# Kernel tuning notes

Measured on AMD Instinct MI355X. Metric: run time of the kernel, lower is better.

Reference implementation:

```python
import jax, jax.numpy as jnp
import numpy as np

N_NODES = 50000
N_EDGES = 800000
N_GRAPHS = 50
D_IN = 128
D_HID = 128
D_OUT = 10


def setup_inputs() -> dict:
    key = jax.random.key(0)
    ks = jax.random.split(key, 8)
    h = jax.random.normal(ks[0], (N_NODES, D_IN), dtype=jnp.float32)
    src = jax.random.randint(ks[1], (N_EDGES,), 0, N_NODES, dtype=jnp.int32)
    dst = jax.random.randint(ks[2], (N_EDGES,), 0, N_NODES, dtype=jnp.int32)
    graph_ids = jnp.sort(jax.random.randint(ks[3], (N_NODES,), 0, N_GRAPHS, dtype=jnp.int32))
    s = 1.0 / np.sqrt(D_HID)
    W1 = jax.random.normal(ks[4], (D_IN, D_HID), dtype=jnp.float32) * s
    W2 = jax.random.normal(ks[5], (D_HID, D_HID), dtype=jnp.float32) * s
    W3 = jax.random.normal(ks[6], (D_HID, D_HID), dtype=jnp.float32) * s
    Wm = jax.random.normal(ks[7], (D_HID, D_OUT), dtype=jnp.float32) * s
    return {
        "h": h, "src": src, "dst": dst, "graph_ids": graph_ids,
        "W1": W1, "b1": jnp.zeros((D_HID,), jnp.float32),
        "W2": W2, "b2": jnp.zeros((D_HID,), jnp.float32),
        "W3": W3, "b3": jnp.zeros((D_HID,), jnp.float32),
        "Wm": Wm, "bm": jnp.zeros((D_OUT,), jnp.float32),
    }


def _graph_conv(h, W, b, src, dst, norm_src, norm_dst):
    # DGL GraphConv, norm='both': out = D_dst^{-1/2} * A @ (D_src^{-1/2} * h) @ W + b
    m = (h * norm_src[:, None])[src]              # [E, d] gather (memory-bound)
    agg = jax.ops.segment_sum(m, dst, num_segments=N_NODES)  # [N, d] scatter-add
    return (agg * norm_dst[:, None]) @ W + b


def reference(h, src, dst, graph_ids, W1, b1, W2, b2, W3, b3, Wm, bm):
    ones_e = jnp.ones((N_EDGES,), jnp.float32)
    out_deg = jax.ops.segment_sum(ones_e, src, num_segments=N_NODES)
    in_deg = jax.ops.segment_sum(ones_e, dst, num_segments=N_NODES)
    norm_src = jnp.clip(out_deg, 1.0, None) ** -0.5
    norm_dst = jnp.clip(in_deg, 1.0, None) ** -0.5

    h = jax.nn.relu(_graph_conv(h, W1, b1, src, dst, norm_src, norm_dst))
    h = jax.nn.relu(_graph_conv(h, W2, b2, src, dst, norm_src, norm_dst))
    h = jax.nn.relu(_graph_conv(h, W3, b3, src, dst, norm_src, norm_dst))

    # mean-nodes readout per graph
    hg_sum = jax.ops.segment_sum(h, graph_ids, num_segments=N_GRAPHS)  # [G, d]
    cnt = jax.ops.segment_sum(jnp.ones((N_NODES,), jnp.float32), graph_ids, num_segments=N_GRAPHS)
    hg = hg_sum / jnp.clip(cnt, 1.0, None)[:, None]

    logits = hg @ Wm + bm                                 # [G, D_OUT]
    return jax.nn.log_softmax(logits, axis=0)             # faithful to dim=0 in source
```

## Files before the change

kernel.cpp:

```cpp
#include <hip/hip_runtime.h>

#define N_NODES 50000
#define N_EDGES 800000
#define N_GRAPHS 50
#define D 128
#define D_OUT 10
#define PLANE_F4 200000
#define NB 196
#define NBLK 196
#define AST 68
#define ZWORDS 50576

__global__ __launch_bounds__(256) void part_hist(const int* __restrict__ dst,
                                                 int* __restrict__ gh,
                                                 int* __restrict__ zbuf) {
    __shared__ int lh[NB];
    int tid = threadIdx.x, blk = blockIdx.x;
    int z = blk * 256 + tid;
    if (z < ZWORDS) zbuf[z] = 0;
    z += 50176;
    if (z < ZWORDS) zbuf[z] = 0;
    if (tid < NB) lh[tid] = 0;
    __syncthreads();
    int base = blk * 4096;
    #pragma unroll
    for (int j = 0; j < 16; j++) {
        int i = base + j * 256 + tid;
        if (i < N_EDGES) atomicAdd(&lh[dst[i] >> 8], 1);
    }
    __syncthreads();
    if (tid < NB) gh[tid * NBLK + blk] = lh[tid];
}

__global__ __launch_bounds__(1024) void part_scan(int* __restrict__ gh, int N) {
    __shared__ int wsum[16];
    __shared__ int carry_s;
    int tid = threadIdx.x;
    int lane = tid & 63, wid = tid >> 6;
    if (tid == 0) carry_s = 0;
    __syncthreads();
    for (int base = 0; base < N; base += 4096) {
        int i0 = base + tid * 4;
        int v0 = (i0 + 0 < N) ? gh[i0 + 0] : 0;
        int v1 = (i0 + 1 < N) ? gh[i0 + 1] : 0;
        int v2 = (i0 + 2 < N) ? gh[i0 + 2] : 0;
        int v3 = (i0 + 3 < N) ? gh[i0 + 3] : 0;
        int s = v0 + v1 + v2 + v3;
        int x = s;
        #pragma unroll
        for (int d = 1; d < 64; d <<= 1) {
            int y = __shfl_up(x, d, 64);
            if (lane >= d) x += y;
        }
        if (lane == 63) wsum[wid] = x;
        __syncthreads();
        if (wid == 0) {
            int t = (lane < 16) ? wsum[lane] : 0;
            #pragma unroll
            for (int d = 1; d < 16; d <<= 1) {
                int y = __shfl_up(t, d, 64);
                if (lane >= d) t += y;
            }
            if (lane < 16) wsum[lane] = t;
        }
        __syncthreads();
        int woff = (wid == 0) ? 0 : wsum[wid - 1];
        int run = carry_s + woff + (x - s);
        if (i0 + 0 < N) gh[i0 + 0] = run; run += v0;
        if (i0 + 1 < N) gh[i0 + 1] = run; run += v1;
        if (i0 + 2 < N) gh[i0 + 2] = run; run += v2;
        if (i0 + 3 < N) gh[i0 + 3] = run; run += v3;
        __syncthreads();
        if (tid == 0) carry_s += wsum[15];
        __syncthreads();
    }
}

__global__ __launch_bounds__(256) void part_scatter(const int* __restrict__ src,
                                                    const int* __restrict__ dst,
                                                    const int* __restrict__ gh,
                                                    unsigned int* __restrict__ packed,
                                                    int* __restrict__ out_deg) {
    __shared__ int lc[NB];
    int tid = threadIdx.x, blk = blockIdx.x;
    if (tid < NB) lc[tid] = gh[tid * NBLK + blk];
    __syncthreads();
    int base = blk * 4096;
    #pragma unroll
    for (int j = 0; j < 16; j++) {
        int i = base + j * 256 + tid;
        if (i < N_EDGES) {
            int d = dst[i];
            int s = src[i];
            atomicAdd(&out_deg[s], 1);
            int p = atomicAdd(&lc[d >> 8], 1);
            packed[p] = ((unsigned int)(d & 255) << 16) | (unsigned int)s;
        }
    }
}

__global__ __launch_bounds__(256) void bucket_csr(const unsigned int* __restrict__ packed,
                                                  const int* __restrict__ gh,
                                                  unsigned short* __restrict__ col16,
                                                  int* __restrict__ row_ptr,
                                                  float* __restrict__ nd,
                                                  int* __restrict__ dhb) {
    __shared__ unsigned int ep[8192];
    __shared__ unsigned short lcol[8192];
    __shared__ int hist[256], cur[256], wsum[4], ldh[64];
    int t = threadIdx.x, b = blockIdx.x;
    int nb = gh[b * NBLK];
    int ne = (b < NB - 1) ? gh[(b + 1) * NBLK] : N_EDGES;
    int cnt = ne - nb;
    if (cnt > 8192) cnt = 8192;
    hist[t] = 0;
    if (t < 64) ldh[t] = 0;
    __syncthreads();
    for (int i = t; i < cnt; i += 256) {
        unsigned int e = packed[nb + i];
        ep[i] = e;
        atomicAdd(&hist[e >> 16], 1);
    }
    __syncthreads();
    int v = hist[t];
    int lane = t & 63, w = t >> 6;
    int x = v;
    #pragma unroll
    for (int d = 1; d < 64; d <<= 1) {
        int y = __shfl_up(x, d, 64);
        if (lane >= d) x += y;
    }
    if (lane == 63) wsum[w] = x;
    __syncthreads();
    int add = 0;
    #pragma unroll
    for (int i = 0; i < 4; i++) if (i < w) add += wsum[i];
    int excl = add + x - v;
    cur[t] = excl;
    int node = b * 256 + t;
    if (node < N_NODES) {
        row_ptr[node] = nb + excl;
        int id = v > 1 ? v : 1;
        nd[node] = 1.0f / sqrtf((float)id);
        atomicAdd(&ldh[v < 63 ? v : 63], 1);
    }
    if (b == NB - 1 && t == 0) row_ptr[N_NODES] = N_EDGES;
    __syncthreads();
    if (t < 64) dhb[t * NBLK + b] = ldh[t];
    for (int i = t; i < cnt; i += 256) {
        unsigned int e = ep[i];
        int p = atomicAdd(&cur[e >> 16], 1);
        lcol[p] = (unsigned short)(e & 0xFFFF);
    }
    __syncthreads();
    for (int i = t; i < cnt; i += 256) col16[nb + i] = lcol[i];
}

__global__ __launch_bounds__(256) void dsort_scatter(const int* __restrict__ row_ptr,
                                                     const int* __restrict__ dhb,
                                                     int* __restrict__ perm) {
    __shared__ int lc[64];
    int t = threadIdx.x, b = blockIdx.x;
    if (t < 64) lc[t] = dhb[t * NBLK + b];
    __syncthreads();
    int n = b * 256 + t;
    if (n < N_NODES) {
        int deg = row_ptr[n + 1] - row_ptr[n];
        int bin = deg < 63 ? deg : 63;
        int pos = atomicAdd(&lc[bin], 1);
        perm[pos] = n;
    }
}

__global__ __launch_bounds__(256) void prescale_k(const float* __restrict__ h,
                                                  const int* __restrict__ out_deg,
                                                  float* __restrict__ out) {
    int i = blockIdx.x * 256 + threadIdx.x;
    if (i < N_NODES * 32) {
        int node = i >> 5;
        int kg = i & 31;
        float4 v = ((const float4*)h)[i];
        int od = out_deg[node];
        float s = 1.0f / sqrtf((float)(od > 1 ? od : 1));
        int p = kg >> 2, q = kg & 3;
        ((float4*)out)[p * PLANE_F4 + node * 4 + q] =
            make_float4(v.x * s, v.y * s, v.z * s, v.w * s);
    }
}

__global__ __launch_bounds__(256) void spmm_k(const float* __restrict__ x,
                                              const int* __restrict__ row_ptr,
                                              const unsigned short* __restrict__ col,
                                              const float* __restrict__ nd,
                                              const int* __restrict__ perm,
                                              float* __restrict__ out) {
    int b = blockIdx.x;
    int slice = b & 7;
    int idx = (b >> 3) * 64 + (threadIdx.x >> 2);
    if (idx >= N_NODES) return;
    int node = perm[idx];
    int q = threadIdx.x & 3;
    int s = row_ptr[node];
    int e = row_ptr[node + 1];
    const float4* xp = (const float4*)x + slice * PLANE_F4;
    float4 a0 = make_float4(0.f, 0.f, 0.f, 0.f);
    float4 a1 = make_float4(0.f, 0.f, 0.f, 0.f);
    float4 a2 = make_float4(0.f, 0.f, 0.f, 0.f);
    float4 a3 = make_float4(0.f, 0.f, 0.f, 0.f);
    int i = s;
    for (; i + 8 <= e; i += 8) {
        int c0 = col[i],     c1 = col[i + 1], c2 = col[i + 2], c3 = col[i + 3];
        int c4 = col[i + 4], c5 = col[i + 5], c6 = col[i + 6], c7 = col[i + 7];
        float4 h0 = xp[c0 * 4 + q];
        float4 h1 = xp[c1 * 4 + q];
        float4 h2 = xp[c2 * 4 + q];
        float4 h3 = xp[c3 * 4 + q];
        float4 h4 = xp[c4 * 4 + q];
        float4 h5 = xp[c5 * 4 + q];
        float4 h6 = xp[c6 * 4 + q];
        float4 h7 = xp[c7 * 4 + q];
        a0.x += h0.x; a0.y += h0.y; a0.z += h0.z; a0.w += h0.w;
        a1.x += h1.x; a1.y += h1.y; a1.z += h1.z; a1.w += h1.w;
        a2.x += h2.x; a2.y += h2.y; a2.z += h2.z; a2.w += h2.w;
        a3.x += h3.x; a3.y += h3.y; a3.z += h3.z; a3.w += h3.w;
        a0.x += h4.x; a0.y += h4.y; a0.z += h4.z; a0.w += h4.w;
        a1.x += h5.x; a1.y += h5.y; a1.z += h5.z; a1.w += h5.w;
        a2.x += h6.x; a2.y += h6.y; a2.z += h6.z; a2.w += h6.w;
        a3.x += h7.x; a3.y += h7.y; a3.z += h7.z; a3.w += h7.w;
    }
    for (; i + 4 <= e; i += 4) {
        int c0 = col[i], c1 = col[i + 1], c2 = col[i + 2], c3 = col[i + 3];
        float4 h0 = xp[c0 * 4 + q];
        float4 h1 = xp[c1 * 4 + q];
        float4 h2 = xp[c2 * 4 + q];
        float4 h3 = xp[c3 * 4 + q];
        a0.x += h0.x; a0.y += h0.y; a0.z += h0.z; a0.w += h0.w;
        a1.x += h1.x; a1.y += h1.y; a1.z += h1.z; a1.w += h1.w;
        a2.x += h2.x; a2.y += h2.y; a2.z += h2.z; a2.w += h2.w;
        a3.x += h3.x; a3.y += h3.y; a3.z += h3.z; a3.w += h3.w;
    }
    for (; i < e; i++) {
        float4 hv = xp[col[i] * 4 + q];
        a0.x += hv.x; a0.y += hv.y; a0.z += hv.z; a0.w += hv.w;
    }
    float ndv = nd[node];
    ((float4*)out)[slice * PLANE_F4 + node * 4 + q] =
        make_float4((a0.x + a1.x + a2.x + a3.x) * ndv,
                    (a0.y + a1.y + a2.y + a3.y) * ndv,
                    (a0.z + a1.z + a2.z + a3.z) * ndv,
                    (a0.w + a1.w + a2.w + a3.w) * ndv);
}

template <int MODE>
__global__ __launch_bounds__(128) void gemm_relu_k(const float* __restrict__ A,
                                                   const float* __restrict__ W,
                                                   const float* __restrict__ bias,
                                                   const int* __restrict__ odeg,
                                                   float* __restrict__ out) {
    __shared__ float As_t[128 * AST];
    int tid = threadIdx.x;
    int row0 = blockIdx.x * 64;
    const float4* A4 = (const float4*)A;
    const float4* W4 = (const float4*)W;

    #pragma unroll
    for (int it = 0; it < 16; it++) {
        int linear = it * 128 + tid;
        int p = linear >> 8;
        int rem = linear & 255;
        int r = rem >> 2;
        int q = rem & 3;
        int row = row0 + r;
        float4 a = (row < N_NODES) ? A4[p * PLANE_F4 + row * 4 + q]
                                   : make_float4(0.f, 0.f, 0.f, 0.f);
        int kb = p * 16 + q * 4;
        As_t[(kb + 0) * AST + r] = a.x;
        As_t[(kb + 1) * AST + r] = a.y;
        As_t[(kb + 2) * AST + r] = a.z;
        As_t[(kb + 3) * AST + r] = a.w;
    }
    __syncthreads();

    int tc = tid & 15;
    int tr = tid >> 4;
    float acc[8][8];
    #pragma unroll
    for (int r = 0; r < 8; r++)
        #pragma unroll
        for (int c = 0; c < 8; c++) acc[r][c] = 0.f;

    const float4* Wp = W4 + tc * 2;
    const float*  Ab = As_t + tr * 8;

    for (int k0 = 0; k0 < 128; k0 += 4) {
        float4 wv0[4], wv1[4], av0[4], av1[4];
        #pragma unroll
        for (int u = 0; u < 4; u++) {
            wv0[u] = Wp[(k0 + u) * 32];
            wv1[u] = Wp[(k0 + u) * 32 + 1];
        }
        #pragma unroll
        for (int u = 0; u < 4; u++) {
            av0[u] = *(const float4*)(Ab + (k0 + u) * AST);
            av1[u] = *(const float4*)(Ab + (k0 + u) * AST + 4);
        }
        #pragma unroll
        for (int u = 0; u < 4; u++) {
            float av[8] = {av0[u].x, av0[u].y, av0[u].z, av0[u].w,
                           av1[u].x, av1[u].y, av1[u].z, av1[u].w};
            float wv[8] = {wv0[u].x, wv0[u].y, wv0[u].z, wv0[u].w,
                           wv1[u].x, wv1[u].y, wv1[u].z, wv1[u].w};
            #pragma unroll
            for (int rr = 0; rr < 8; rr++)
                #pragma unroll
                for (int cc = 0; cc < 8; cc++)
                    acc[rr][cc] = fmaf(av[rr], wv[cc], acc[rr][cc]);
        }
    }

    float4 bv0 = ((const float4*)bias)[tc * 2];
    float4 bv1 = ((const float4*)bias)[tc * 2 + 1];
    #pragma unroll
    for (int rr = 0; rr < 8; rr++) {
        int row = row0 + tr * 8 + rr;
        if (row < N_NODES) {
            float4 o0, o1;
            o0.x = fmaxf(acc[rr][0] + bv0.x, 0.f);
            o0.y = fmaxf(acc[rr][1] + bv0.y, 0.f);
            o0.z = fmaxf(acc[rr][2] + bv0.z, 0.f);
            o0.w = fmaxf(acc[rr][3] + bv0.w, 0.f);
            o1.x = fmaxf(acc[rr][4] + bv1.x, 0.f);
            o1.y = fmaxf(acc[rr][5] + bv1.y, 0.f);
            o1.z = fmaxf(acc[rr][6] + bv1.z, 0.f);
            o1.w = fmaxf(acc[rr][7] + bv1.w, 0.f);
            if (MODE == 0) {
                int od = odeg[row];
                float s = 1.0f / sqrtf((float)(od > 1 ? od : 1));
                o0.x *= s; o0.y *= s; o0.z *= s; o0.w *= s;
                o1.x *= s; o1.y *= s; o1.z *= s; o1.w *= s;
                int p = tc >> 1;
                int q0 = (tc & 1) * 2;
                ((float4*)out)[p * PLANE_F4 + row * 4 + q0] = o0;
                ((float4*)out)[p * PLANE_F4 + row * 4 + q0 + 1] = o1;
            } else {
                ((float4*)out)[row * 32 + tc * 2] = o0;
                ((float4*)out)[row * 32 + tc * 2 + 1] = o1;
            }
        }
    }
}

__global__ __launch_bounds__(256) void proj_readout_k(const float* __restrict__ h,
                                                      const int* __restrict__ gid,
                                                      const float* __restrict__ Wm,
                                                      float* __restrict__ hgp,
                                                      int* __restrict__ gcnt) {
    __shared__ float Wmt[10 * 144];
    int tid = threadIdx.x;
    for (int i = tid; i < 1280; i += 256) {
        int k = i / 10, o = i % 10;
        Wmt[o * 144 + k + 4 * (k >> 5)] = Wm[i];
    }
    __syncthreads();

    int v = blockIdx.x * 64 + (tid >> 2);
    int quarter = tid & 3;
    int lane = tid & 63;

    float acc[D_OUT];
    #pragma unroll
    for (int o = 0; o < D_OUT; o++) acc[o] = 0.f;
    int g = -1;
    int cnt = 0;
    if (v < N_NODES) {
        g = gid[v];
        cnt = (quarter == 0) ? 1 : 0;
        const float4* h4 = (const float4*)h + v * 32 + quarter * 8;
        const float* wbase = Wmt + quarter * 36;
        #pragma unroll
        for (int kk = 0; kk < 8; kk++) {
            float4 hv = h4[kk];
            #pragma unroll
            for (int o = 0; o < D_OUT; o++) {
                float4 w = *(const float4*)(wbase + o * 144 + kk * 4);
                acc[o] += hv.x * w.x + hv.y * w.y + hv.z * w.z + hv.w * w.w;
            }
        }
    }

    #pragma unroll
    for (int d = 1; d < 64; d <<= 1) {
        int gp = __shfl_up(g, d, 64);
        int cp = __shfl_up(cnt, d, 64);
        bool take = (lane >= d) && (gp == g);
        #pragma unroll
        for (int o = 0; o < D_OUT; o++) {
            float ap = __shfl_up(acc[o], d, 64);
            if (take) acc[o] += ap;
        }
        if (take) cnt += cp;
    }
    int gn = __shfl_down(g, 1, 64);
    bool tail = (lane == 63) || (gn != g);
    if (tail && g >= 0) {
        #pragma unroll
        for (int o = 0; o < D_OUT; o++) atomicAdd(&hgp[g * D_OUT + o], acc[o]);
        if (cnt > 0) atomicAdd(&gcnt[g], cnt);
    }
}

__global__ __launch_bounds__(512) void final_k(const float* __restrict__ hgp,
                                               const int* __restrict__ gcnt,
                                               const float* __restrict__ bm,
                                               float* __restrict__ out) {
    __shared__ float lg[N_GRAPHS * D_OUT];
    __shared__ float colm[D_OUT], colls[D_OUT];
    int tid = threadIdx.x;
    if (tid < N_GRAPHS * D_OUT) {
        int g = tid / D_OUT, o = tid % D_OUT;
        float c = (float)gcnt[g];
        lg[tid] = hgp[tid] / (c > 1.f ? c : 1.f) + bm[o];
    }
    __syncthreads();
    if (tid < D_OUT) {
        float m = -1e30f;
        for (int g = 0; g < N_GRAPHS; g++) m = fmaxf(m, lg[g * D_OUT + tid]);
        float s = 0.f;
        for (int g = 0; g < N_GRAPHS; g++) s += expf(lg[g * D_OUT + tid] - m);
        colm[tid] = m; colls[tid] = logf(s);
    }
    __syncthreads();
    if (tid < N_GRAPHS * D_OUT) {
        int o = tid % D_OUT;
        out[tid] = lg[tid] - colm[o] - colls[o];
    }
}

extern "C" void kernel_launch(void* const* d_in, const int* in_sizes, int n_in,
                              void* d_out, int out_size, void* d_ws, size_t ws_size,
                              hipStream_t stream) {
    const float* h_in = (const float*)d_in[0];
    const int*   src  = (const int*)d_in[1];
    const int*   dst  = (const int*)d_in[2];
    const int*   gid  = (const int*)d_in[3];
    const float* W1 = (const float*)d_in[4];  const float* b1 = (const float*)d_in[5];
    const float* W2 = (const float*)d_in[6];  const float* b2 = (const float*)d_in[7];
    const float* W3 = (const float*)d_in[8];  const float* b3 = (const float*)d_in[9];
    const float* Wm = (const float*)d_in[10]; const float* bm = (const float*)d_in[11];

    char* ws = (char*)d_ws;
    int*            row_ptr = (int*)(ws + 0);
    unsigned short* col16   = (unsigned short*)(ws + 200032);
    float*          nd      = (float*)(ws + 1800032);
    int*            out_deg = (int*)(ws + 2000032);
    int*            gcnt    = (int*)(ws + 2200032);
    float*          hgp     = (float*)(ws + 2200288);
    int*            gh      = (int*)(ws + 2202336);
    int*            dhb     = (int*)(ws + 2356000);
    int*            perm    = (int*)(ws + 2406176);
    float*          bufA    = (float*)(ws + 2606176);
    float*          bufB    = (float*)(ws + 28206176);
    unsigned int*   packed  = (unsigned int*)bufB;

    part_hist<<<NBLK, 256, 0, stream>>>(dst, gh, out_deg);
    part_scan<<<1, 1024, 0, stream>>>(gh, NB * NBLK);
    part_scatter<<<NBLK, 256, 0, stream>>>(src, dst, gh, packed, out_deg);
    bucket_csr<<<NB, 256, 0, stream>>>(packed, gh, col16, row_ptr, nd, dhb);
    part_scan<<<1, 1024, 0, stream>>>(dhb, 64 * NBLK);
    dsort_scatter<<<196, 256, 0, stream>>>(row_ptr, dhb, perm);
    prescale_k<<<6250, 256, 0, stream>>>(h_in, out_deg, bufA);

    spmm_k<<<6256, 256, 0, stream>>>(bufA, row_ptr, col16, nd, perm, bufB);
    gemm_relu_k<0><<<782, 128, 0, stream>>>(bufB, W1, b1, out_deg, bufA);
    spmm_k<<<6256, 256, 0, stream>>>(bufA, row_ptr, col16, nd, perm, bufB);
    gemm_relu_k<0><<<782, 128, 0, stream>>>(bufB, W2, b2, out_deg, bufA);
    spmm_k<<<6256, 256, 0, stream>>>(bufA, row_ptr, col16, nd, perm, bufB);
    gemm_relu_k<1><<<782, 128, 0, stream>>>(bufB, W3, b3, out_deg, bufA);

    proj_readout_k<<<782, 256, 0, stream>>>(bufA, gid, Wm, hgp, gcnt);
    final_k<<<1, 512, 0, stream>>>(hgp, gcnt, bm, (float*)d_out);
}
```

Measured before the change: 525.6 us.

## Reorder CSR columns into degree-sorted order and stage them in LDS for SpMM

Adds a second row pointer array built by scanning per-position degrees in the degree-sorted permutation order. A new col_reorder kernel rewrites the column indices so each 64-row SpMM block reads a contiguous span. spmm_k now loads that span into shared memory cooperatively before gathering, and falls back to global reads when the span exceeds the LDS capacity. It also recomputes the dst norm from the degree instead of loading nd. The cost is two extra preprocessing launches (a scan and the reorder) plus an LDS staging pass and a barrier in each SpMM block.

```diff
diff --git a/kernel.cpp b/kernel.cpp
--- a/kernel.cpp
+++ b/kernel.cpp
@@ -9,6 +9,7 @@
 #define NB 196
 #define NBLK 196
 #define AST 68
+#define LCOL_CAP 3072
 #define ZWORDS 50576
 
 __global__ __launch_bounds__(256) void part_hist(const int* __restrict__ dst,
@@ -103,7 +104,6 @@
                                                   const int* __restrict__ gh,
                                                   unsigned short* __restrict__ col16,
                                                   int* __restrict__ row_ptr,
-                                                  float* __restrict__ nd,
                                                   int* __restrict__ dhb) {
     __shared__ unsigned int ep[8192];
     __shared__ unsigned short lcol[8192];
@@ -140,8 +140,6 @@
     int node = b * 256 + t;
     if (node < N_NODES) {
         row_ptr[node] = nb + excl;
-        int id = v > 1 ? v : 1;
-        nd[node] = 1.0f / sqrtf((float)id);
         atomicAdd(&ldh[v < 63 ? v : 63], 1);
     }
     if (b == NB - 1 && t == 0) row_ptr[N_NODES] = N_EDGES;
@@ -158,7 +156,10 @@
 
 __global__ __launch_bounds__(256) void dsort_scatter(const int* __restrict__ row_ptr,
                                                      const int* __restrict__ dhb,
-                                                     int* __restrict__ perm) {
+                                                     int* __restrict__ perm,
+                                                     int* __restrict__ row_ptr2,
+                                                     const unsigned int* __restrict__ col_u,
+                                                     unsigned int* __restrict__ cscr) {
     __shared__ int lc[64];
     int t = threadIdx.x, b = blockIdx.x;
     if (t < 64) lc[t] = dhb[t * NBLK + b];
@@ -169,7 +170,25 @@
         int bin = deg < 63 ? deg : 63;
         int pos = atomicAdd(&lc[bin], 1);
         perm[pos] = n;
-    }
+        row_ptr2[pos] = deg;
+    }
+    int gtid = b * 256 + t;
+    for (int i = gtid; i < N_EDGES / 2; i += NBLK * 256) cscr[i] = col_u[i];
+}
+
+__global__ __launch_bounds__(256) void col_reorder(const int* __restrict__ row_ptr,
+                                                   const int* __restrict__ row_ptr2,
+                                                   const int* __restrict__ perm,
+                                                   const unsigned short* __restrict__ cscr,
+                                                   unsigned short* __restrict__ col16) {
+    int idx = blockIdx.x * 64 + (threadIdx.x >> 2);
+    if (idx >= N_NODES) return;
+    int lane = threadIdx.x & 3;
+    int node = perm[idx];
+    int s = row_ptr[node];
+    int len = row_ptr[node + 1] - s;
+    int d2 = row_ptr2[idx];
+    for (int j = lane; j < len; j += 4) col16[d2 + j] = cscr[s + j];
 }
 
 __global__ __launch_bounds__(256) void prescale_k(const float* __restrict__ h,
@@ -189,61 +208,93 @@
 }
 
 __global__ __launch_bounds__(256) void spmm_k(const float* __restrict__ x,
-                                              const int* __restrict__ row_ptr,
+                                              const int* __restrict__ row_ptr2,
                                               const unsigned short* __restrict__ col,
-                                              const float* __restrict__ nd,
                                               const int* __restrict__ perm,
                                               float* __restrict__ out) {
+    __shared__ unsigned short lcol[LCOL_CAP];
     int b = blockIdx.x;
     int slice = b & 7;
-    int idx = (b >> 3) * 64 + (threadIdx.x >> 2);
+    int i0b = (b >> 3) * 64;
+    int iendb = i0b + 64; if (iendb > N_NODES) iendb = N_NODES;
+    int e0 = row_ptr2[i0b];
+    int e1 = row_ptr2[iendb];
+    int span = e1 - e0;
+    int staged = span < LCOL_CAP ? span : LCOL_CAP;
+    for (int j = threadIdx.x; j < staged; j += 256) lcol[j] = col[e0 + j];
+    __syncthreads();
+
+    int idx = i0b + (threadIdx.x >> 2);
     if (idx >= N_NODES) return;
+    int q = threadIdx.x & 3;
+    int s = row_ptr2[idx];
+    int e = row_ptr2[idx + 1];
     int node = perm[idx];
-    int q = threadIdx.x & 3;
-    int s = row_ptr[node];
-    int e = row_ptr[node + 1];
     const float4* xp = (const float4*)x + slice * PLANE_F4;
     float4 a0 = make_float4(0.f, 0.f, 0.f, 0.f);
     float4 a1 = make_float4(0.f, 0.f, 0.f, 0.f);
     float4 a2 = make_float4(0.f, 0.f, 0.f, 0.f);
     float4 a3 = make_float4(0.f, 0.f, 0.f, 0.f);
-    int i = s;
-    for (; i + 8 <= e; i += 8) {
-        int c0 = col[i],     c1 = col[i + 1], c2 = col[i + 2], c3 = col[i + 3];
-        int c4 = col[i + 4], c5 = col[i + 5], c6 = col[i + 6], c7 = col[i + 7];
-        float4 h0 = xp[c0 * 4 + q];
-        float4 h1 = xp[c1 * 4 + q];
-        float4 h2 = xp[c2 * 4 + q];
-        float4 h3 = xp[c3 * 4 + q];
-        float4 h4 = xp[c4 * 4 + q];
-        float4 h5 = xp[c5 * 4 + q];
-        float4 h6 = xp[c6 * 4 + q];
-        float4 h7 = xp[c7 * 4 + q];
-        a0.x += h0.x; a0.y += h0.y; a0.z += h0.z; a0.w += h0.w;
-        a1.x += h1.x; a1.y += h1.y; a1.z += h1.z; a1.w += h1.w;
-        a2.x += h2.x; a2.y += h2.y; a2.z += h2.z; a2.w += h2.w;
-        a3.x += h3.x; a3.y += h3.y; a3.z += h3.z; a3.w += h3.w;
-        a0.x += h4.x; a0.y += h4.y; a0.z += h4.z; a0.w += h4.w;
-        a1.x += h5.x; a1.y += h5.y; a1.z += h5.z; a1.w += h5.w;
-        a2.x += h6.x; a2.y += h6.y; a2.z += h6.z; a2.w += h6.w;
-        a3.x += h7.x; a3.y += h7.y; a3.z += h7.z; a3.w += h7.w;
-    }
-    for (; i + 4 <= e; i += 4) {
-        int c0 = col[i], c1 = col[i + 1], c2 = col[i + 2], c3 = col[i + 3];
-        float4 h0 = xp[c0 * 4 + q];
-        float4 h1 = xp[c1 * 4 + q];
-        float4 h2 = xp[c2 * 4 + q];
-        float4 h3 = xp[c3 * 4 + q];
-        a0.x += h0.x; a0.y += h0.y; a0.z += h0.z; a0.w += h0.w;
-        a1.x += h1.x; a1.y += h1.y; a1.z += h1.z; a1.w += h1.w;
-        a2.x += h2.x; a2.y += h2.y; a2.z += h2.z; a2.w += h2.w;
-        a3.x += h3.x; a3.y += h3.y; a3.z += h3.z; a3.w += h3.w;
-    }
-    for (; i < e; i++) {
-        float4 hv = xp[col[i] * 4 + q];
-        a0.x += hv.x; a0.y += hv.y; a0.z += hv.z; a0.w += hv.w;
-    }
-    float ndv = nd[node];
+
+    if (e - e0 <= staged) {
+        const unsigned short* lc = lcol + (s - e0);
+        int n = e - s;
+        int i = 0;
+        for (; i + 8 <= n; i += 8) {
+            int c0 = lc[i],     c1 = lc[i + 1], c2 = lc[i + 2], c3 = lc[i + 3];
+            int c4 = lc[i + 4], c5 = lc[i + 5], c6 = lc[i + 6], c7 = lc[i + 7];
+            float4 h0 = xp[c0 * 4 + q];
+            float4 h1 = xp[c1 * 4 + q];
+            float4 h2 = xp[c2 * 4 + q];
+            float4 h3 = xp[c3 * 4 + q];
+            float4 h4 = xp[c4 * 4 + q];
+            float4 h5 = xp[c5 * 4 + q];
+            float4 h6 = xp[c6 * 4 + q];
+            float4 h7 = xp[c7 * 4 + q];
+            a0.x += h0.x; a0.y += h0.y; a0.z += h0.z; a0.w += h0.w;
+            a1.x += h1.x; a1.y += h1.y; a1.z += h1.z; a1.w += h1.w;
+            a2.x += h2.x; a2.y += h2.y; a2.z += h2.z; a2.w += h2.w;
+            a3.x += h3.x; a3.y += h3.y; a3.z += h3.z; a3.w += h3.w;
+            a0.x += h4.x; a0.y += h4.y; a0.z += h4.z; a0.w += h4.w;
+            a1.x += h5.x; a1.y += h5.y; a1.z += h5.z; a1.w += h5.w;
+            a2.x += h6.x; a2.y += h6.y; a2.z += h6.z; a2.w += h6.w;
+            a3.x += h7.x; a3.y += h7.y; a3.z += h7.z; a3.w += h7.w;
+        }
+        for (; i + 4 <= n; i += 4) {
+            int c0 = lc[i], c1 = lc[i + 1], c2 = lc[i + 2], c3 = lc[i + 3];
+            float4 h0 = xp[c0 * 4 + q];
+            float4 h1 = xp[c1 * 4 + q];
+            float4 h2 = xp[c2 * 4 + q];
+            float4 h3 = xp[c3 * 4 + q];
+            a0.x += h0.x; a0.y += h0.y; a0.z += h0.z; a0.w += h0.w;
+            a1.x += h1.x; a1.y += h1.y; a1.z += h1.z; a1.w += h1.w;
+            a2.x += h2.x; a2.y += h2.y; a2.z += h2.z; a2.w += h2.w;
+            a3.x += h3.x; a3.y += h3.y; a3.z += h3.z; a3.w += h3.w;
+        }
+        for (; i < n; i++) {
+            float4 hv = xp[lc[i] * 4 + q];
+            a0.x += hv.x; a0.y += hv.y; a0.z += hv.z; a0.w += hv.w;
+        }
+    } else {
+        int i = s;
+        for (; i + 4 <= e; i += 4) {
+            int c0 = col[i], c1 = col[i + 1], c2 = col[i + 2], c3 = col[i + 3];
+            float4 h0 = xp[c0 * 4 + q];
+            float4 h1 = xp[c1 * 4 + q];
+            float4 h2 = xp[c2 * 4 + q];
+            float4 h3 = xp[c3 * 4 + q];
+            a0.x += h0.x; a0.y += h0.y; a0.z += h0.z; a0.w += h0.w;
+            a1.x += h1.x; a1.y += h1.y; a1.z += h1.z; a1.w += h1.w;
+            a2.x += h2.x; a2.y += h2.y; a2.z += h2.z; a2.w += h2.w;
+            a3.x += h3.x; a3.y += h3.y; a3.z += h3.z; a3.w += h3.w;
+        }
+        for (; i < e; i++) {
+            float4 hv = xp[col[i] * 4 + q];
+            a0.x += hv.x; a0.y += hv.y; a0.z += hv.z; a0.w += hv.w;
+        }
+    }
+    int deg = e - s;
+    float ndv = 1.0f / sqrtf((float)(deg > 1 ? deg : 1));
     ((float4*)out)[slice * PLANE_F4 + node * 4 + q] =
         make_float4((a0.x + a1.x + a2.x + a3.x) * ndv,
                     (a0.y + a1.y + a2.y + a3.y) * ndv,
@@ -449,32 +500,37 @@
     const float* Wm = (const float*)d_in[10]; const float* bm = (const float*)d_in[11];
 
     char* ws = (char*)d_ws;
-    int*            row_ptr = (int*)(ws + 0);
-    unsigned short* col16   = (unsigned short*)(ws + 200032);
-    float*          nd      = (float*)(ws + 1800032);
-    int*            out_deg = (int*)(ws + 2000032);
-    int*            gcnt    = (int*)(ws + 2200032);
-    float*          hgp     = (float*)(ws + 2200288);
-    int*            gh      = (int*)(ws + 2202336);
-    int*            dhb     = (int*)(ws + 2356000);
-    int*            perm    = (int*)(ws + 2406176);
-    float*          bufA    = (float*)(ws + 2606176);
-    float*          bufB    = (float*)(ws + 28206176);
-    unsigned int*   packed  = (unsigned int*)bufB;
+    int*            row_ptr  = (int*)(ws + 0);
+    unsigned short* col16    = (unsigned short*)(ws + 200032);
+    int*            row_ptr2 = (int*)(ws + 1800032);
+    int*            out_deg  = (int*)(ws + 2000064);
+    int*            gcnt     = (int*)(ws + 2200064);
+    float*          hgp      = (float*)(ws + 2200320);
+    int*            gh       = (int*)(ws + 2202368);
+    int*            dhb      = (int*)(ws + 2356032);
+    int*            perm     = (int*)(ws + 2406208);
+    float*          bufA     = (float*)(ws + 2606208);
+    float*          bufB     = (float*)(ws + 28206208);
+    unsigned int*   packed   = (unsigned int*)bufB;
+    unsigned int*   cscr     = (unsigned int*)bufB;
 
     part_hist<<<NBLK, 256, 0, stream>>>(dst, gh, out_deg);
     part_scan<<<1, 1024, 0, stream>>>(gh, NB * NBLK);
     part_scatter<<<NBLK, 256, 0, stream>>>(src, dst, gh, packed, out_deg);
-    bucket_csr<<<NB, 256, 0, stream>>>(packed, gh, col16, row_ptr, nd, dhb);
+    bucket_csr<<<NB, 256, 0, stream>>>(packed, gh, col16, row_ptr, dhb);
     part_scan<<<1, 1024, 0, stream>>>(dhb, 64 * NBLK);
-    dsort_scatter<<<196, 256, 0, stream>>>(row_ptr, dhb, perm);
+    dsort_scatter<<<NBLK, 256, 0, stream>>>(row_ptr, dhb, perm, row_ptr2,
+                                            (const unsigned int*)col16, cscr);
+    part_scan<<<1, 1024, 0, stream>>>(row_ptr2, N_NODES + 1);
+    col_reorder<<<782, 256, 0, stream>>>(row_ptr, row_ptr2, perm,
+                                         (const unsigned short*)cscr, col16);
     prescale_k<<<6250, 256, 0, stream>>>(h_in, out_deg, bufA);
 
-    spmm_k<<<6256, 256, 0, stream>>>(bufA, row_ptr, col16, nd, perm, bufB);
+    spmm_k<<<6256, 256, 0, stream>>>(bufA, row_ptr2, col16, perm, bufB);
     gemm_relu_k<0><<<782, 128, 0, stream>>>(bufB, W1, b1, out_deg, bufA);
-    spmm_k<<<6256, 256, 0, stream>>>(bufA, row_ptr, col16, nd, perm, bufB);
+    spmm_k<<<6256, 256, 0, stream>>>(bufA, row_ptr2, col16, perm, bufB);
     gemm_relu_k<0><<<782, 128, 0, stream>>>(bufB, W2, b2, out_deg, bufA);
-    spmm_k<<<6256, 256, 0, stream>>>(bufA, row_ptr, col16, nd, perm, bufB);
+    spmm_k<<<6256, 256, 0, stream>>>(bufA, row_ptr2, col16, perm, bufB);
     gemm_relu_k<1><<<782, 128, 0, stream>>>(bufB, W3, b3, out_deg, bufA);
 
     proj_readout_k<<<782, 256, 0, stream>>>(bufA, gid, Wm, hgp, gcnt);
```

Measured after the change: 475.8 us. -9.5%, faster.
